# Optimization experiments

Measured on AMD Instinct MI355X. Metric: run time of the kernel, lower is better.

The kernel has to match this reference:

```python
import jax, jax.numpy as jnp
import numpy as np

KERNEL_SIZE = 13
SIGMA_MIN, SIGMA_MAX = 0.4, 10.0
BETA, THRESHOLD = 0.95, 1.0


@jax.custom_vjp
def spike(x):
    # Heaviside forward, snntorch ATan surrogate backward (alpha=2)
    return (x > 0).astype(x.dtype)

def _spike_fwd(x):
    return spike(x), x

def _spike_bwd(x, g):
    return (g / (1.0 + (jnp.pi * x) ** 2),)

spike.defvjp(_spike_fwd, _spike_bwd)


def setup_inputs() -> dict:
    key = jax.random.key(0)
    k1, k2 = jax.random.split(key)
    B, C, T = 32, 224, 2048
    inp = jax.random.normal(k1, (B, 1, C, T), dtype=jnp.float32)
    linear_w = jax.random.normal(k2, (1, C), dtype=jnp.float32) * (1.0 / np.sqrt(C))
    return {"inp": inp, "linear_w": linear_w}


def _forward(inp, linear_w):
    x = inp[:, 0]  # [B, C, T]
    B, C, T = x.shape
    sigma_mean = 0.5 * (SIGMA_MIN + SIGMA_MAX)
    # adaptive sigma per (batch, time): Linear over channel axis, no bias
    w = sigma_mean + jnp.einsum('bct,c->bt', x, linear_w[0]) * (SIGMA_MAX - SIGMA_MIN)
    w = jnp.clip(w, SIGMA_MIN, SIGMA_MAX)  # [B, T]

    half = KERNEL_SIZE // 2
    r = jnp.linspace(-half, half, KERNEL_SIZE)
    r_all = jnp.linspace(-half * 10, half * 10, KERNEL_SIZE * 10)
    sig = w[..., None]  # [B, T, 1]
    kern = jnp.exp(-0.5 * (r / sig) ** 2)                       # [B, T, K]
    norm = jnp.exp(-0.5 * (r_all / sig) ** 2).sum(-1, keepdims=True)
    kern = kern / norm                                          # normalized over fine grid

    # adaptive gaussian smoothing along the CHANNEL axis (per timestep kernel)
    xt = jnp.transpose(x, (0, 2, 1))                            # [B, T, C]
    padded = jnp.pad(xt, ((0, 0), (0, 0), (half, half)))        # zero pad channels
    x_mean = sum(padded[:, :, k:k + C] * kern[:, :, k:k + 1]
                 for k in range(KERNEL_SIZE))                   # [B, T, C]
    x_mean = jnp.transpose(x_mean, (0, 2, 1))                   # [B, C, T]

    I = x - jax.nn.relu(x - x_mean)                             # soft min(x, x_mean)

    # Leaky-integrate-and-fire over time (snntorch Leaky, reset-by-subtract)
    def step(mem, I_t):
        reset = jax.lax.stop_gradient((mem > THRESHOLD).astype(I_t.dtype))
        mem = BETA * mem + I_t - reset * THRESHOLD
        spk = spike(mem - THRESHOLD)
        return mem, spk

    I_seq = jnp.transpose(I, (2, 0, 1))                         # [T, B, C]
    _, spk = jax.lax.scan(step, jnp.zeros((B, C), I.dtype), I_seq)
    spk = jnp.transpose(spk, (1, 2, 0))                         # [B, C, T]
    return spk[:, None]                                         # [B, 1, C, T]


def reference(inp, linear_w):
    return _forward(inp, linear_w)
```

## Files before the change

kernel.cpp:

```cpp
#include <hip/hip_runtime.h>
#include <math.h>

#define BB 32
#define CCH 224
#define TTT 2048
#define BT (BB*TTT)
#define TPB 64
#define NT  (TTT/TPB)
#define CG  28
#define NCG (CCH/CG)
#define IROW 29

#define PF(s,h) ((s)*2+(h))
#define CF(s)   (4+(s))
#define SF(s)   (6+(s))
#define OF(s,h) (8+(s)*2+(h))

__global__ __launch_bounds__(256) void kw(
    const float* __restrict__ x, const float* __restrict__ lw,
    double* __restrict__ kernG)
{
    __shared__ double sd[4][256];
    __shared__ float  lws[CCH];
    const int b   = blockIdx.y;
    const int t0  = blockIdx.x * 256;
    const int tid = threadIdx.x;

    if (tid < CCH) lws[tid] = lw[tid];
    __syncthreads();

    {
        const int q = tid & 63, m = tid >> 6;
        const float* xb = x + (((size_t)(b * CCH + 56 * m)) << 11) + t0 + 4 * q;
        double a0 = 0, a1 = 0, a2 = 0, a3 = 0;
        #pragma unroll 8
        for (int i = 0; i < 56; ++i) {
            float4 v = *(const float4*)(xb + ((size_t)i << 11));
            double wv = (double)lws[56 * m + i];
            a0 += (double)v.x * wv;
            a1 += (double)v.y * wv;
            a2 += (double)v.z * wv;
            a3 += (double)v.w * wv;
        }
        sd[m][4 * q + 0] = a0; sd[m][4 * q + 1] = a1;
        sd[m][4 * q + 2] = a2; sd[m][4 * q + 3] = a3;
    }
    __syncthreads();

    {
        double s2 = (sd[0][tid] + sd[1][tid]) + (sd[2][tid] + sd[3][tid]);

        double w = 5.2 + s2 * 9.6;
        w = fmin(fmax(w, 0.4), 10.0);
        double iw2 = 1.0 / (w * w);

        const double s = 120.0 / 129.0;
        double G  = exp(-0.125 * s * s * iw2);
        double G2 = G * G, G4 = G2 * G2, G8 = G4 * G4;
        double term = G, cmul = G8, norm = G;
        for (int u = 1; u <= 64; ++u) { term *= cmul; cmul *= G8; norm += term; }
        norm *= 2.0;

        double P = exp(-0.5 * iw2), P2 = P * P;
        double a = 1.0, bm = P, inv = 1.0 / norm;
        double* kr = kernG + (size_t)b * TTT + t0 + tid;
        kr[0] = inv;
        #pragma unroll
        for (int d = 1; d <= 6; ++d) {
            a *= bm; bm *= P2;
            kr[(size_t)d * BT] = a * inv;
        }
    }
}

__global__ __launch_bounds__(192) void kf(
    const float* __restrict__ x, const double* __restrict__ kernG,
    float* __restrict__ out)
{
    __shared__ double Is[2][TPB][IROW];
    __shared__ unsigned long long bitsb[2][CG];
    __shared__ int fl[16];

    const int b    = blockIdx.y;
    const int c0   = blockIdx.x * CG;
    const int tid  = threadIdx.x;
    const int wid  = tid >> 6;
    const int lane = tid & 63;

    if (tid < 16) fl[tid] = 0;
    __syncthreads();

    const float*  xbase = x + (((size_t)(b * CCH)) << 11);
    const double* kbase = kernG + (size_t)b * TTT;
    float* obase = out + (((size_t)(b * CCH + c0)) << 11);

    if (wid >= 1) {
        const int h  = wid - 1;
        const int cb = 14 * h;
        const int crow0 = c0 + cb - 6;
        float  xc[26], xn[26];
        double kc[7],  kn[7];

        #pragma unroll
        for (int i = 0; i < 26; ++i) {
            int cr = crow0 + i;
            xc[i] = (cr >= 0 && cr < CCH) ? xbase[((size_t)cr << 11) + lane] : 0.0f;
        }
        #pragma unroll
        for (int d = 0; d < 7; ++d) kc[d] = kbase[(size_t)d * BT + lane];

        #pragma unroll 1
        for (int k = 0; k <= NT + 1; ++k) {
            if (k + 1 <= NT - 1) {
                const int gt = (k + 1) * TPB + lane;
                #pragma unroll
                for (int i = 0; i < 26; ++i) {
                    int cr = crow0 + i;
                    xn[i] = (cr >= 0 && cr < CCH) ? xbase[((size_t)cr << 11) + gt] : 0.0f;
                }
                #pragma unroll
                for (int d = 0; d < 7; ++d) kn[d] = kbase[(size_t)d * BT + gt];
            }
            if (k <= NT - 1) {
                const int s = k & 1;
                while (__hip_atomic_load(&fl[CF(s)], __ATOMIC_ACQUIRE,
                                         __HIP_MEMORY_SCOPE_WORKGROUP) < k - 1)
                    __builtin_amdgcn_s_sleep(1);
                #pragma unroll
                for (int c = 0; c < 14; ++c) {
                    double acc = 0.0;
                    #pragma unroll
                    for (int kk = 0; kk < 13; ++kk) {
                        int d = kk < 6 ? 6 - kk : kk - 6;
                        acc = fma((double)xc[c + kk], kc[d], acc);
                    }
                    double xvv = (double)xc[c + 6];
                    double dd  = xvv - acc;
                    Is[s][lane][cb + c] = xvv - (dd > 0.0 ? dd : 0.0);
                }
                if (lane == 0)
                    __hip_atomic_store(&fl[PF(s, h)], k + 1, __ATOMIC_RELEASE,
                                       __HIP_MEMORY_SCOPE_WORKGROUP);
            }
            const int j = k - 2;
            if (j >= 0) {
                const int s2 = j & 1;
                while (__hip_atomic_load(&fl[SF(s2)], __ATOMIC_ACQUIRE,
                                         __HIP_MEMORY_SCOPE_WORKGROUP) < j + 1)
                    __builtin_amdgcn_s_sleep(1);
                unsigned long long bb[4];
                #pragma unroll
                for (int i = 0; i < 4; ++i) {
                    int e = lane + (i << 6);
                    int cl = (e < 224) ? (e >> 4) : 13;
                    bb[i] = bitsb[s2][cb + cl];
                }
                if (lane == 0)
                    __hip_atomic_store(&fl[OF(s2, h)], j + 1, __ATOMIC_RELEASE,
                                       __HIP_MEMORY_SCOPE_WORKGROUP);
                #pragma unroll
                for (int i = 0; i < 4; ++i) {
                    int e = lane + (i << 6);
                    if (e < 224) {
                        int cl = e >> 4, qq = e & 15;
                        unsigned long long bv = bb[i] >> (4 * qq);
                        float4 v;
                        v.x = (bv & 1ull) ? 1.0f : 0.0f;
                        v.y = (bv & 2ull) ? 1.0f : 0.0f;
                        v.z = (bv & 4ull) ? 1.0f : 0.0f;
                        v.w = (bv & 8ull) ? 1.0f : 0.0f;
                        *(float4*)(obase + ((size_t)(cb + cl) << 11) + j * TPB + 4 * qq) = v;
                    }
                }
            }
            if (k + 1 <= NT - 1) {
                #pragma unroll
                for (int i = 0; i < 26; ++i) xc[i] = xn[i];
                #pragma unroll
                for (int d = 0; d < 7; ++d) kc[d] = kn[d];
            }
        }
    } else {
        const int c    = lane;
        const int cidx = (c < CG) ? c : 0;
        double mem = 0.0;
        bool   r   = false;

        #pragma unroll 1
        for (int k = 0; k < NT; ++k) {
            const int s = k & 1;
            while (__hip_atomic_load(&fl[PF(s, 0)], __ATOMIC_ACQUIRE,
                                     __HIP_MEMORY_SCOPE_WORKGROUP) < k + 1 ||
                   __hip_atomic_load(&fl[PF(s, 1)], __ATOMIC_ACQUIRE,
                                     __HIP_MEMORY_SCOPE_WORKGROUP) < k + 1)
                __builtin_amdgcn_s_sleep(1);

            unsigned long long bits = 0ull;
            {
                double va[8], vb[8];
                #pragma unroll
                for (int j2 = 0; j2 < 8; ++j2) va[j2] = Is[s][j2][cidx];
                #pragma unroll
                for (int g = 0; g < 64; g += 16) {
                    #pragma unroll
                    for (int j2 = 0; j2 < 8; ++j2) vb[j2] = Is[s][g + 8 + j2][cidx];
                    #pragma unroll
                    for (int j2 = 0; j2 < 8; ++j2) {
                        double a2 = va[j2];
                        double cm = a2 - 1.0;
                        double m1 = fma(0.95, mem, a2);
                        double m2 = fma(0.95, mem, cm);
                        mem = r ? m2 : m1;
                        r = mem > 1.0;
                        bits |= (unsigned long long)(r ? 1 : 0) << (g + j2);
                    }
                    if (g + 16 < 64) {
                        #pragma unroll
                        for (int j2 = 0; j2 < 8; ++j2) va[j2] = Is[s][g + 16 + j2][cidx];
                    }
                    #pragma unroll
                    for (int j2 = 0; j2 < 8; ++j2) {
                        double a2 = vb[j2];
                        double cm = a2 - 1.0;
                        double m1 = fma(0.95, mem, a2);
                        double m2 = fma(0.95, mem, cm);
                        mem = r ? m2 : m1;
                        r = mem > 1.0;
                        bits |= (unsigned long long)(r ? 1 : 0) << (g + 8 + j2);
                    }
                }
            }
            if (lane == 0)
                __hip_atomic_store(&fl[CF(s)], k + 1, __ATOMIC_RELEASE,
                                   __HIP_MEMORY_SCOPE_WORKGROUP);

            const int s2 = k & 1;
            while (__hip_atomic_load(&fl[OF(s2, 0)], __ATOMIC_ACQUIRE,
                                     __HIP_MEMORY_SCOPE_WORKGROUP) < k - 1 ||
                   __hip_atomic_load(&fl[OF(s2, 1)], __ATOMIC_ACQUIRE,
                                     __HIP_MEMORY_SCOPE_WORKGROUP) < k - 1)
                __builtin_amdgcn_s_sleep(1);
            if (c < CG) bitsb[s2][c] = bits;
            if (lane == 0)
                __hip_atomic_store(&fl[SF(s2)], k + 1, __ATOMIC_RELEASE,
                                   __HIP_MEMORY_SCOPE_WORKGROUP);
        }
    }
}

extern "C" void kernel_launch(void* const* d_in, const int* in_sizes, int n_in,
                              void* d_out, int out_size, void* d_ws, size_t ws_size,
                              hipStream_t stream)
{
    const float* x  = (const float*)d_in[0];
    const float* lw = (const float*)d_in[1];
    float* out = (float*)d_out;

    double* kernG = (double*)d_ws;

    kw<<<dim3(TTT / 256, BB), 256, 0, stream>>>(x, lw, kernG);
    kf<<<dim3(NCG, BB), 192, 0, stream>>>(x, kernG, out);
}
```

Baseline: 174.3 us.

## Add dedicated output-writer wave, deepen ring buffer, and retile sigma kernel

```diff
diff --git a/kernel.cpp b/kernel.cpp
--- a/kernel.cpp
+++ b/kernel.cpp
@@ -10,45 +10,44 @@
 #define CG  28
 #define NCG (CCH/CG)
 #define IROW 29
-
-#define PF(s,h) ((s)*2+(h))
-#define CF(s)   (4+(s))
-#define SF(s)   (6+(s))
-#define OF(s,h) (8+(s)*2+(h))
+#define RD 4
 
 __global__ __launch_bounds__(256) void kw(
     const float* __restrict__ x, const float* __restrict__ lw,
     double* __restrict__ kernG)
 {
-    __shared__ double sd[4][256];
+    __shared__ double sd[16][64];
     __shared__ float  lws[CCH];
     const int b   = blockIdx.y;
-    const int t0  = blockIdx.x * 256;
+    const int t0  = blockIdx.x * 64;
     const int tid = threadIdx.x;
 
     if (tid < CCH) lws[tid] = lw[tid];
     __syncthreads();
 
     {
-        const int q = tid & 63, m = tid >> 6;
-        const float* xb = x + (((size_t)(b * CCH + 56 * m)) << 11) + t0 + 4 * q;
+        const int q = tid & 15, g = tid >> 4;
+        const float* xb = x + (((size_t)(b * CCH + g * 14)) << 11) + t0 + 4 * q;
         double a0 = 0, a1 = 0, a2 = 0, a3 = 0;
-        #pragma unroll 8
-        for (int i = 0; i < 56; ++i) {
+        #pragma unroll
+        for (int i = 0; i < 14; ++i) {
             float4 v = *(const float4*)(xb + ((size_t)i << 11));
-            double wv = (double)lws[56 * m + i];
+            double wv = (double)lws[g * 14 + i];
             a0 += (double)v.x * wv;
             a1 += (double)v.y * wv;
             a2 += (double)v.z * wv;
             a3 += (double)v.w * wv;
         }
-        sd[m][4 * q + 0] = a0; sd[m][4 * q + 1] = a1;
-        sd[m][4 * q + 2] = a2; sd[m][4 * q + 3] = a3;
+        sd[g][4 * q + 0] = a0; sd[g][4 * q + 1] = a1;
+        sd[g][4 * q + 2] = a2; sd[g][4 * q + 3] = a3;
     }
     __syncthreads();
 
-    {
-        double s2 = (sd[0][tid] + sd[1][tid]) + (sd[2][tid] + sd[3][tid]);
+    if (tid < 64) {
+        const int t = tid;
+        double s2 = 0.0;
+        #pragma unroll
+        for (int g = 0; g < 16; ++g) s2 += sd[g][t];
 
         double w = 5.2 + s2 * 9.6;
         w = fmin(fmax(w, 0.4), 10.0);
@@ -63,7 +62,7 @@
 
         double P = exp(-0.5 * iw2), P2 = P * P;
         double a = 1.0, bm = P, inv = 1.0 / norm;
-        double* kr = kernG + (size_t)b * TTT + t0 + tid;
+        double* kr = kernG + (size_t)b * TTT + t0 + t;
         kr[0] = inv;
         #pragma unroll
         for (int d = 1; d <= 6; ++d) {
@@ -73,13 +72,18 @@
     }
 }
 
-__global__ __launch_bounds__(192) void kf(
+#define PF(h,s) ((h)*RD+(s))
+#define CF(s)   (8+(s))
+#define SF(s)   (12+(s))
+#define OW(s)   (16+(s))
+
+__global__ __launch_bounds__(256) void kf(
     const float* __restrict__ x, const double* __restrict__ kernG,
     float* __restrict__ out)
 {
-    __shared__ double Is[2][TPB][IROW];
-    __shared__ unsigned long long bitsb[2][CG];
-    __shared__ int fl[16];
+    __shared__ double Is[RD][TPB][IROW];
+    __shared__ unsigned long long bitsb[RD][CG];
+    __shared__ int fl[32];
 
     const int b    = blockIdx.y;
     const int c0   = blockIdx.x * CG;
@@ -87,14 +91,14 @@
     const int wid  = tid >> 6;
     const int lane = tid & 63;
 
-    if (tid < 16) fl[tid] = 0;
+    if (tid < 32) fl[tid] = 0;
     __syncthreads();
 
     const float*  xbase = x + (((size_t)(b * CCH)) << 11);
     const double* kbase = kernG + (size_t)b * TTT;
     float* obase = out + (((size_t)(b * CCH + c0)) << 11);
 
-    if (wid >= 1) {
+    if (wid == 1 || wid == 2) {
         const int h  = wid - 1;
         const int cb = 14 * h;
         const int crow0 = c0 + cb - 6;
@@ -110,8 +114,8 @@
         for (int d = 0; d < 7; ++d) kc[d] = kbase[(size_t)d * BT + lane];
 
         #pragma unroll 1
-        for (int k = 0; k <= NT + 1; ++k) {
-            if (k + 1 <= NT - 1) {
+        for (int k = 0; k < NT; ++k) {
+            if (k + 1 < NT) {
                 const int gt = (k + 1) * TPB + lane;
                 #pragma unroll
                 for (int i = 0; i < 26; ++i) {
@@ -121,66 +125,36 @@
                 #pragma unroll
                 for (int d = 0; d < 7; ++d) kn[d] = kbase[(size_t)d * BT + gt];
             }
-            if (k <= NT - 1) {
-                const int s = k & 1;
-                while (__hip_atomic_load(&fl[CF(s)], __ATOMIC_ACQUIRE,
-                                         __HIP_MEMORY_SCOPE_WORKGROUP) < k - 1)
-                    __builtin_amdgcn_s_sleep(1);
-                #pragma unroll
-                for (int c = 0; c < 14; ++c) {
-                    double acc = 0.0;
-                    #pragma unroll
-                    for (int kk = 0; kk < 13; ++kk) {
-                        int d = kk < 6 ? 6 - kk : kk - 6;
-                        acc = fma((double)xc[c + kk], kc[d], acc);
-                    }
-                    double xvv = (double)xc[c + 6];
-                    double dd  = xvv - acc;
-                    Is[s][lane][cb + c] = xvv - (dd > 0.0 ? dd : 0.0);
-                }
-                if (lane == 0)
-                    __hip_atomic_store(&fl[PF(s, h)], k + 1, __ATOMIC_RELEASE,
-                                       __HIP_MEMORY_SCOPE_WORKGROUP);
-            }
-            const int j = k - 2;
-            if (j >= 0) {
-                const int s2 = j & 1;
-                while (__hip_atomic_load(&fl[SF(s2)], __ATOMIC_ACQUIRE,
-                                         __HIP_MEMORY_SCOPE_WORKGROUP) < j + 1)
-                    __builtin_amdgcn_s_sleep(1);
-                unsigned long long bb[4];
-                #pragma unroll
-                for (int i = 0; i < 4; ++i) {
-                    int e = lane + (i << 6);
-                    int cl = (e < 224) ? (e >> 4) : 13;
-                    bb[i] = bitsb[s2][cb + cl];
-                }
-                if (lane == 0)
-                    __hip_atomic_store(&fl[OF(s2, h)], j + 1, __ATOMIC_RELEASE,
-                                       __HIP_MEMORY_SCOPE_WORKGROUP);
-                #pragma unroll
-                for (int i = 0; i < 4; ++i) {
-                    int e = lane + (i << 6);
-                    if (e < 224) {
-                        int cl = e >> 4, qq = e & 15;
-                        unsigned long long bv = bb[i] >> (4 * qq);
-                        float4 v;
-                        v.x = (bv & 1ull) ? 1.0f : 0.0f;
-                        v.y = (bv & 2ull) ? 1.0f : 0.0f;
-                        v.z = (bv & 4ull) ? 1.0f : 0.0f;
-                        v.w = (bv & 8ull) ? 1.0f : 0.0f;
-                        *(float4*)(obase + ((size_t)(cb + cl) << 11) + j * TPB + 4 * qq) = v;
-                    }
-                }
-            }
-            if (k + 1 <= NT - 1) {
+            double iv[14];
+            #pragma unroll
+            for (int c = 0; c < 14; ++c) {
+                double acc = 0.0;
+                #pragma unroll
+                for (int kk = 0; kk < 13; ++kk) {
+                    int d = kk < 6 ? 6 - kk : kk - 6;
+                    acc = fma((double)xc[c + kk], kc[d], acc);
+                }
+                double xvv = (double)xc[c + 6];
+                double dd  = xvv - acc;
+                iv[c] = xvv - (dd > 0.0 ? dd : 0.0);
+            }
+            const int s = k & (RD - 1);
+            while (__hip_atomic_load(&fl[CF(s)], __ATOMIC_ACQUIRE,
+                                     __HIP_MEMORY_SCOPE_WORKGROUP) < k + 1 - RD)
+                __builtin_amdgcn_s_sleep(1);
+            #pragma unroll
+            for (int c = 0; c < 14; ++c) Is[s][lane][cb + c] = iv[c];
+            if (lane == 0)
+                __hip_atomic_store(&fl[PF(h, s)], k + 1, __ATOMIC_RELEASE,
+                                   __HIP_MEMORY_SCOPE_WORKGROUP);
+            if (k + 1 < NT) {
                 #pragma unroll
                 for (int i = 0; i < 26; ++i) xc[i] = xn[i];
                 #pragma unroll
                 for (int d = 0; d < 7; ++d) kc[d] = kn[d];
             }
         }
-    } else {
+    } else if (wid == 0) {
         const int c    = lane;
         const int cidx = (c < CG) ? c : 0;
         double mem = 0.0;
@@ -188,45 +162,47 @@
 
         #pragma unroll 1
         for (int k = 0; k < NT; ++k) {
-            const int s = k & 1;
-            while (__hip_atomic_load(&fl[PF(s, 0)], __ATOMIC_ACQUIRE,
+            const int s = k & (RD - 1);
+            while (__hip_atomic_load(&fl[PF(0, s)], __ATOMIC_ACQUIRE,
                                      __HIP_MEMORY_SCOPE_WORKGROUP) < k + 1 ||
-                   __hip_atomic_load(&fl[PF(s, 1)], __ATOMIC_ACQUIRE,
+                   __hip_atomic_load(&fl[PF(1, s)], __ATOMIC_ACQUIRE,
                                      __HIP_MEMORY_SCOPE_WORKGROUP) < k + 1)
                 __builtin_amdgcn_s_sleep(1);
 
             unsigned long long bits = 0ull;
             {
-                double va[8], vb[8];
-                #pragma unroll
-                for (int j2 = 0; j2 < 8; ++j2) va[j2] = Is[s][j2][cidx];
+                double va[8], vam[8], vb[8], vbm[8];
+                #pragma unroll
+                for (int j = 0; j < 8; ++j) {
+                    va[j] = Is[s][j][cidx]; vam[j] = va[j] - 1.0;
+                }
                 #pragma unroll
                 for (int g = 0; g < 64; g += 16) {
                     #pragma unroll
-                    for (int j2 = 0; j2 < 8; ++j2) vb[j2] = Is[s][g + 8 + j2][cidx];
+                    for (int j = 0; j < 8; ++j) {
+                        vb[j] = Is[s][g + 8 + j][cidx]; vbm[j] = vb[j] - 1.0;
+                    }
                     #pragma unroll
-                    for (int j2 = 0; j2 < 8; ++j2) {
-                        double a2 = va[j2];
-                        double cm = a2 - 1.0;
-                        double m1 = fma(0.95, mem, a2);
-                        double m2 = fma(0.95, mem, cm);
+                    for (int j = 0; j < 8; ++j) {
+                        double m1 = fma(0.95, mem, va[j]);
+                        double m2 = fma(0.95, mem, vam[j]);
                         mem = r ? m2 : m1;
                         r = mem > 1.0;
-                        bits |= (unsigned long long)(r ? 1 : 0) << (g + j2);
+                        bits |= (unsigned long long)(r ? 1 : 0) << (g + j);
                     }
                     if (g + 16 < 64) {
                         #pragma unroll
-                        for (int j2 = 0; j2 < 8; ++j2) va[j2] = Is[s][g + 16 + j2][cidx];
+                        for (int j = 0; j < 8; ++j) {
+                            va[j] = Is[s][g + 16 + j][cidx]; vam[j] = va[j] - 1.0;
+                        }
                     }
                     #pragma unroll
-                    for (int j2 = 0; j2 < 8; ++j2) {
-                        double a2 = vb[j2];
-                        double cm = a2 - 1.0;
-                        double m1 = fma(0.95, mem, a2);
-                        double m2 = fma(0.95, mem, cm);
+                    for (int j = 0; j < 8; ++j) {
+                        double m1 = fma(0.95, mem, vb[j]);
+                        double m2 = fma(0.95, mem, vbm[j]);
                         mem = r ? m2 : m1;
                         r = mem > 1.0;
-                        bits |= (unsigned long long)(r ? 1 : 0) << (g + 8 + j2);
+                        bits |= (unsigned long long)(r ? 1 : 0) << (g + 8 + j);
                     }
                 }
             }
@@ -234,16 +210,42 @@
                 __hip_atomic_store(&fl[CF(s)], k + 1, __ATOMIC_RELEASE,
                                    __HIP_MEMORY_SCOPE_WORKGROUP);
 
-            const int s2 = k & 1;
-            while (__hip_atomic_load(&fl[OF(s2, 0)], __ATOMIC_ACQUIRE,
-                                     __HIP_MEMORY_SCOPE_WORKGROUP) < k - 1 ||
-                   __hip_atomic_load(&fl[OF(s2, 1)], __ATOMIC_ACQUIRE,
-                                     __HIP_MEMORY_SCOPE_WORKGROUP) < k - 1)
-                __builtin_amdgcn_s_sleep(1);
-            if (c < CG) bitsb[s2][c] = bits;
-            if (lane == 0)
-                __hip_atomic_store(&fl[SF(s2)], k + 1, __ATOMIC_RELEASE,
-                                   __HIP_MEMORY_SCOPE_WORKGROUP);
+            while (__hip_atomic_load(&fl[OW(s)], __ATOMIC_ACQUIRE,
+                                     __HIP_MEMORY_SCOPE_WORKGROUP) < k + 1 - RD)
+                __builtin_amdgcn_s_sleep(1);
+            if (c < CG) bitsb[s][c] = bits;
+            if (lane == 0)
+                __hip_atomic_store(&fl[SF(s)], k + 1, __ATOMIC_RELEASE,
+                                   __HIP_MEMORY_SCOPE_WORKGROUP);
+        }
+    } else {
+        const int qq = lane & 15;
+        #pragma unroll 1
+        for (int k = 0; k < NT; ++k) {
+            const int s = k & (RD - 1);
+            while (__hip_atomic_load(&fl[SF(s)], __ATOMIC_ACQUIRE,
+                                     __HIP_MEMORY_SCOPE_WORKGROUP) < k + 1)
+                __builtin_amdgcn_s_sleep(1);
+            unsigned long long bb[7];
+            #pragma unroll
+            for (int i = 0; i < 7; ++i) {
+                int cc = (lane >> 4) + 4 * i;
+                bb[i] = bitsb[s][cc];
+            }
+            if (lane == 0)
+                __hip_atomic_store(&fl[OW(s)], k + 1, __ATOMIC_RELEASE,
+                                   __HIP_MEMORY_SCOPE_WORKGROUP);
+            #pragma unroll
+            for (int i = 0; i < 7; ++i) {
+                int cc = (lane >> 4) + 4 * i;
+                unsigned long long bv = bb[i] >> (4 * qq);
+                float4 v;
+                v.x = (bv & 1ull) ? 1.0f : 0.0f;
+                v.y = (bv & 2ull) ? 1.0f : 0.0f;
+                v.z = (bv & 4ull) ? 1.0f : 0.0f;
+                v.w = (bv & 8ull) ? 1.0f : 0.0f;
+                *(float4*)(obase + ((size_t)cc << 11) + k * TPB + 4 * qq) = v;
+            }
         }
     }
 }
@@ -258,6 +260,6 @@
 
     double* kernG = (double*)d_ws;
 
-    kw<<<dim3(TTT / 256, BB), 256, 0, stream>>>(x, lw, kernG);
-    kf<<<dim3(NCG, BB), 192, 0, stream>>>(x, kernG, out);
+    kw<<<dim3(TTT / 64, BB), 256, 0, stream>>>(x, lw, kernG);
+    kf<<<dim3(NCG, BB), 256, 0, stream>>>(x, kernG, out);
 }
```

After: 157.5 us. 9.6% less time.
